# Kernel tuning notes

Measured on AMD Instinct MI355X. Metric: run time of the kernel, lower is better.

## Reference

```python
import jax, jax.numpy as jnp
import numpy as np

B, S, D, H = 2, 2048, 1024, 16
HD = D // H  # head_dim = 64


def setup_inputs() -> dict:
    key = jax.random.key(0)
    k1, k2, k3 = jax.random.split(key, 3)
    x = jax.random.normal(k1, (B, S, D), dtype=jnp.float32)
    mask = jnp.zeros((B, S, S), dtype=jnp.float32)  # additive mask
    # Dense(3*D) params (glorot-ish scale) and Dense(D) output projection
    Wqkv = jax.random.normal(k2, (D, 3 * D), dtype=jnp.float32) * (1.0 / np.sqrt(D))
    bqkv = jnp.zeros((3 * D,), dtype=jnp.float32)
    Wo = jax.random.normal(k3, (D, D), dtype=jnp.float32) * (1.0 / np.sqrt(D))
    bo = jnp.zeros((D,), dtype=jnp.float32)
    return {"x": x, "mask": mask, "Wqkv": Wqkv, "bqkv": bqkv, "Wo": Wo, "bo": bo}


def reference(x, mask, Wqkv, bqkv, Wo, bo):
    b, s, d = x.shape
    qkv = x @ Wqkv + bqkv                              # [B,S,3D]
    qkv = qkv.reshape(b, s, H, 3 * HD).transpose(0, 2, 1, 3)  # [B,H,S,3*HD]
    q, k, v = jnp.split(qkv, 3, axis=-1)               # each [B,H,S,HD]
    scale = 1.0 / jnp.sqrt(jnp.float32(HD))
    scores = jnp.einsum('bhqd,bhkd->bhqk', q, k) * scale  # [B,H,S,S]
    scores = scores + mask[:, None, :, :]
    attn = jax.nn.softmax(scores, axis=-1)
    values = jnp.einsum('bhqk,bhkd->bhqd', attn, v)    # [B,H,S,HD]
    # Faithful to original: reshape WITHOUT transposing heads back
    values = values.reshape(b, s, H * HD)              # [B,S,D]
    return values @ Wo + bo
```

## Files before the change

### kernel.cpp

```cpp
#include <hip/hip_runtime.h>
#include <hip/hip_bf16.h>

#define B_ 2
#define S_ 2048
#define D_ 1024
#define H_ 16
#define HD_ 64

typedef __attribute__((ext_vector_type(8))) short short8;
typedef __attribute__((ext_vector_type(4))) float f32x4;
typedef __attribute__((ext_vector_type(16))) float f32x16;
typedef __attribute__((ext_vector_type(4))) unsigned short us4;

static __device__ __forceinline__ ushort f2bf(float x) {
  __hip_bfloat16 h = __float2bfloat16(x);
  return *reinterpret_cast<ushort*>(&h);
}

static __device__ __forceinline__ void gld_lds16(void* lds, const void* g) {
  __builtin_amdgcn_global_load_lds(
      (__attribute__((address_space(1))) void*)(g),
      (__attribute__((address_space(3))) void*)(lds), 16, 0, 0);
}


__global__ __launch_bounds__(256) void cvt_bf16_vec(const float4* __restrict__ in,
                                                    ushort* __restrict__ out, int n4) {
  int i = blockIdx.x * blockDim.x + threadIdx.x;
  if (i < n4) {
    float4 v = in[i];
    ushort4 o;
    o.x = f2bf(v.x); o.y = f2bf(v.y); o.z = f2bf(v.z); o.w = f2bf(v.w);
    *reinterpret_cast<ushort4*>(out + (size_t)i * 4) = o;
  }
}

__global__ __launch_bounds__(256) void transpose_cvt(const float* __restrict__ in,
                                                     ushort* __restrict__ out,
                                                     int K, int N) {
  __shared__ float tile[32][33];
  const int bn = blockIdx.x * 32, bk = blockIdx.y * 32;
  const int tx = threadIdx.x, ty = threadIdx.y;
  #pragma unroll
  for (int i = ty; i < 32; i += 8)
    tile[i][tx] = in[(size_t)(bk + i) * N + bn + tx];
  __syncthreads();
  #pragma unroll
  for (int i = ty; i < 32; i += 8)
    out[(size_t)(bn + i) * K + bk + tx] = f2bf(tile[tx][i]);
}

template <bool OUT_BF16>
__global__ __launch_bounds__(256) void gemm_bt(const ushort* __restrict__ A,
                                               const ushort* __restrict__ Bt,
                                               const float* __restrict__ bias,
                                               ushort* __restrict__ Cb,
                                               float* __restrict__ Cf,
                                               int M, int N, int K) {
  __shared__ __align__(16) ushort As[128 * 32];
  __shared__ __align__(16) ushort Bs[128 * 32];
  const int tid = threadIdx.x;
  const int lane = tid & 63, wid = tid >> 6;
  const int wr = wid >> 1, wc = wid & 1;
  const int row0 = blockIdx.x * 128, col0 = blockIdx.y * 128;
  const int l15 = lane & 15, lhi = lane >> 4;

  f32x4 acc[4][4];
  #pragma unroll
  for (int i = 0; i < 4; ++i)
    #pragma unroll
    for (int j = 0; j < 4; ++j)
      acc[i][j] = f32x4{0.f, 0.f, 0.f, 0.f};

  const int sr = tid >> 2;
  const int scol = (tid & 3) * 8;

  for (int k0 = 0; k0 < K; k0 += 32) {
    gld_lds16(&As[(size_t)tid * 8],        &A[(size_t)(row0 + sr) * K + k0 + scol]);
    gld_lds16(&As[2048 + (size_t)tid * 8], &A[(size_t)(row0 + 64 + sr) * K + k0 + scol]);
    gld_lds16(&Bs[(size_t)tid * 8],        &Bt[(size_t)(col0 + sr) * K + k0 + scol]);
    gld_lds16(&Bs[2048 + (size_t)tid * 8], &Bt[(size_t)(col0 + 64 + sr) * K + k0 + scol]);
    __syncthreads();

    short8 af[4], bfr[4];
    #pragma unroll
    for (int mt = 0; mt < 4; ++mt)
      af[mt] = *(const short8*)&As[(wr * 64 + mt * 16 + l15) * 32 + lhi * 8];
    #pragma unroll
    for (int nt = 0; nt < 4; ++nt)
      bfr[nt] = *(const short8*)&Bs[(wc * 64 + nt * 16 + l15) * 32 + lhi * 8];
    #pragma unroll
    for (int mt = 0; mt < 4; ++mt)
      #pragma unroll
      for (int nt = 0; nt < 4; ++nt)
        acc[mt][nt] = __builtin_amdgcn_mfma_f32_16x16x32_bf16(af[mt], bfr[nt], acc[mt][nt], 0, 0, 0);
    __syncthreads();
  }

  const int orow = row0 + wr * 64;
  const int ocol = col0 + wc * 64 + l15;
  #pragma unroll
  for (int mt = 0; mt < 4; ++mt) {
    #pragma unroll
    for (int nt = 0; nt < 4; ++nt) {
      const int gc = ocol + nt * 16;
      const float bv = bias[gc];
      #pragma unroll
      for (int r = 0; r < 4; ++r) {
        const int gr = orow + mt * 16 + lhi * 4 + r;
        const float v = acc[mt][nt][r] + bv;
        if (OUT_BF16) Cb[(size_t)gr * N + gc] = f2bf(v);
        else          Cf[(size_t)gr * N + gc] = v;
      }
    }
  }
}

__global__ __launch_bounds__(256, 2) void flash_attn(const ushort* __restrict__ qkv,
                                                     const float* __restrict__ mask,
                                                     ushort* __restrict__ values) {
  __shared__ __align__(16) ushort Ks[2][64 * 64];
  __shared__ __align__(16) ushort Vt[2][64 * 64];

  const int tid = threadIdx.x;
  const int lane = tid & 63, wid = tid >> 6;
  const int l31 = lane & 31, lhalf = lane >> 5;
  const int qt = blockIdx.x, bh = blockIdx.y, b = bh >> 4, h = bh & 15;
  const size_t base = (size_t)b * S_ * 3072 + (size_t)h * 192;
  const int q = qt * 128 + wid * 32 + l31;
  const int NT = S_ / 64;

  short8 qf[4];
  {
    const ushort* qrow = qkv + base + (size_t)q * 3072 + lhalf * 8;
    qf[0] = *(const short8*)(qrow);
    qf[1] = *(const short8*)(qrow + 16);
    qf[2] = *(const short8*)(qrow + 32);
    qf[3] = *(const short8*)(qrow + 48);
  }

  const int srow = tid >> 3, sch = tid & 7;
  const int hsr = (srow ^ (srow >> 3)) & 7;
  const int scs = sch ^ hsr;
  const int kg = tid & 15, d0 = (tid >> 4) * 4;
  const int skg = (kg & 12) | ((kg & 1) << 1) | ((kg >> 1) & 1);

  float m_run = -3.0e38f, l_run = 0.f;
  f32x16 o[2];
  #pragma unroll
  for (int dg = 0; dg < 2; ++dg)
    #pragma unroll
    for (int i = 0; i < 16; ++i) o[dg][i] = 0.f;

  const float* mrow = mask + ((size_t)b * S_ + q) * S_;
  us4 vr[4];
  f32x16 scA[2], scB[2];

#define QKT_(SCDST, KSBUF)                                                     \
  {                                                                            \
    _Pragma("unroll")                                                          \
    for (int g = 0; g < 2; ++g) {                                              \
      const int row_ = g * 32 + l31;                                           \
      const int hk_ = (row_ ^ (row_ >> 3)) & 7;                                \
      const ushort* kp_ = &(KSBUF)[row_ * 64];                                 \
      f32x16 s_;                                                               \
      _Pragma("unroll")                                                        \
      for (int i = 0; i < 16; ++i) s_[i] = 0.f;                                \
      _Pragma("unroll")                                                        \
      for (int kd = 0; kd < 4; ++kd) {                                         \
        short8 kf_ = *(const short8*)&kp_[(((kd * 2 + lhalf) ^ hk_) & 7) * 8]; \
        s_ = __builtin_amdgcn_mfma_f32_32x32x16_bf16(kf_, qf[kd], s_, 0, 0, 0);\
      }                                                                        \
      (SCDST)[g] = s_;                                                         \
    }                                                                          \
  }

#define VSCATTER_(VTBUF)                                                       \
  {                                                                            \
    _Pragma("unroll")                                                          \
    for (int dd = 0; dd < 4; ++dd) {                                           \
      const int d_ = d0 + dd;                                                  \
      const int hd_ = (d_ ^ (d_ >> 3)) & 7;                                    \
      us4 w_;                                                                  \
      w_[0] = vr[0][dd]; w_[1] = vr[1][dd];                                    \
      w_[2] = vr[2][dd]; w_[3] = vr[3][dd];                                    \
      *(us4*)&(VTBUF)[d_ * 64 + (((skg >> 1) ^ hd_) & 7) * 8 + (skg & 1) * 4] = w_; \
    }                                                                          \
  }

#define HALF_(T, SCCUR, SCNEXT)                                                \
  {                                                                            \
    const int t_ = (T);                                                        \
    const bool pre1_ = (t_ + 1 < NT), pre2_ = (t_ + 2 < NT);                   \
    if (pre2_) {                                                               \
      const ushort* kn_ = qkv + base + (size_t)(t_ + 2) * 64 * 3072 +          \
                          (size_t)srow * 3072 + 64;                            \
      gld_lds16(&Ks[t_ & 1][tid * 8],        kn_ + scs * 8);                   \
      gld_lds16(&Ks[t_ & 1][2048 + tid * 8], kn_ + (size_t)32 * 3072 + (scs ^ 4) * 8); \
    }                                                                          \
    if (pre1_) {                                                               \
      const ushort* vn_ = qkv + base + (size_t)(t_ + 1) * 64 * 3072 + 128 + d0;\
      _Pragma("unroll")                                                        \
      for (int kk = 0; kk < 4; ++kk)                                           \
        vr[kk] = *(const us4*)(vn_ + (size_t)(kg * 4 + kk) * 3072);            \
    }                                                                          \
    f32x4 mk_[8];                                                              \
    {                                                                          \
      const float* mp_ = mrow + t_ * 64 + lhalf * 4;                           \
      _Pragma("unroll")                                                        \
      for (int i = 0; i < 8; ++i)                                              \
        mk_[i] = *(const f32x4*)(mp_ + (i >> 2) * 32 + (i & 3) * 8);           \
    }                                                                          \
    __builtin_amdgcn_s_setprio(1);                                             \
    if (pre1_) QKT_(SCNEXT, Ks[(t_ + 1) & 1]);                                 \
                     \
    _Pragma("unroll")                                                          \
    for (int g = 0; g < 2; ++g)                                                \
      _Pragma("unroll")                                                        \
      for (int r = 0; r < 16; ++r)                                             \
        (SCCUR)[g][r] = (SCCUR)[g][r] * 0.125f + mk_[g * 4 + (r >> 2)][r & 3]; \
    float mx_ = (SCCUR)[0][0];                                                 \
    _Pragma("unroll")                                                          \
    for (int g = 0; g < 2; ++g)                                                \
      _Pragma("unroll")                                                        \
      for (int r = 0; r < 16; ++r) mx_ = fmaxf(mx_, (SCCUR)[g][r]);            \
    mx_ = fmaxf(mx_, __shfl_xor(mx_, 32));                                     \
    if (__any(mx_ > m_run + 8.0f)) {                                           \
      const float mnew_ = fmaxf(m_run, mx_);                                   \
      const float alpha_ = __expf(m_run - mnew_);                              \
      m_run = mnew_;                                                           \
      l_run *= alpha_;                                                         \
      _Pragma("unroll")                                                        \
      for (int dg = 0; dg < 2; ++dg)                                           \
        _Pragma("unroll")                                                      \
        for (int i = 0; i < 16; ++i) o[dg][i] *= alpha_;                       \
    }                                                                          \
    float ps_ = 0.f;                                                           \
    _Pragma("unroll")                                                          \
    for (int g = 0; g < 2; ++g)                                                \
      _Pragma("unroll")                                                        \
      for (int r = 0; r < 16; ++r) {                                           \
        const float p_ = __expf((SCCUR)[g][r] - m_run);                        \
        (SCCUR)[g][r] = p_;                                                    \
        ps_ += p_;                                                             \
      }                                                                        \
    ps_ += __shfl_xor(ps_, 32);                                                \
    l_run += ps_;                                                              \
    short8 pf_[4];                                                             \
    _Pragma("unroll")                                                          \
    for (int ks = 0; ks < 4; ++ks)                                             \
      _Pragma("unroll")                                                        \
      for (int j = 0; j < 8; ++j)                                              \
        pf_[ks][j] = (short)f2bf((SCCUR)[ks >> 1][8 * (ks & 1) + j]);          \
    _Pragma("unroll")                                                          \
    for (int dg = 0; dg < 2; ++dg) {                                           \
      const int d_ = dg * 32 + l31;                                            \
      const int hv_ = (d_ ^ (d_ >> 3)) & 7;                                    \
      const ushort* vp_ = &Vt[t_ & 1][d_ * 64];                                \
      _Pragma("unroll")                                                        \
      for (int ks = 0; ks < 4; ++ks) {                                         \
        short8 vf_ = *(const short8*)&vp_[(((ks * 2 + lhalf) ^ hv_) & 7) * 8]; \
        o[dg] = __builtin_amdgcn_mfma_f32_32x32x16_bf16(vf_, pf_[ks], o[dg], 0, 0, 0); \
      }                                                                        \
    }                                                                          \
    __builtin_amdgcn_s_setprio(0);                                             \
    if (pre1_) VSCATTER_(Vt[(t_ + 1) & 1]);                                    \
    __syncthreads();                                                           \
  }

  {
    const ushort* k0 = qkv + base + (size_t)srow * 3072 + 64;
    gld_lds16(&Ks[0][tid * 8],        k0 + scs * 8);
    gld_lds16(&Ks[0][2048 + tid * 8], k0 + (size_t)32 * 3072 + (scs ^ 4) * 8);
    const ushort* k1 = k0 + (size_t)64 * 3072;
    gld_lds16(&Ks[1][tid * 8],        k1 + scs * 8);
    gld_lds16(&Ks[1][2048 + tid * 8], k1 + (size_t)32 * 3072 + (scs ^ 4) * 8);
    #pragma unroll
    for (int kk = 0; kk < 4; ++kk)
      vr[kk] = *(const us4*)(qkv + base + (size_t)(kg * 4 + kk) * 3072 + 128 + d0);
    VSCATTER_(Vt[0]);
    __syncthreads();
    QKT_(scA, Ks[0]);
  }

  for (int tp = 0; tp < NT; tp += 2) {
    HALF_(tp,     scA, scB);
    HALF_(tp + 1, scB, scA);
  }

  const float inv = 1.0f / l_run;
  ushort* vout = values + ((size_t)bh * S_ + q) * 64;
  #pragma unroll
  for (int dg = 0; dg < 2; ++dg)
    #pragma unroll
    for (int quad = 0; quad < 4; ++quad) {
      us4 w;
      #pragma unroll
      for (int r = 0; r < 4; ++r) w[r] = f2bf(o[dg][quad * 4 + r] * inv);
      *(us4*)(vout + dg * 32 + quad * 8 + lhalf * 4) = w;
    }
#undef HALF_
#undef VSCATTER_
#undef QKT_
}


extern "C" void kernel_launch(void* const* d_in, const int* in_sizes, int n_in,
                              void* d_out, int out_size, void* d_ws, size_t ws_size,
                              hipStream_t stream) {
  const float* x    = (const float*)d_in[0];
  const float* mask = (const float*)d_in[1];
  const float* Wqkv = (const float*)d_in[2];
  const float* bqkv = (const float*)d_in[3];
  const float* Wo   = (const float*)d_in[4];
  const float* bo   = (const float*)d_in[5];
  float* out = (float*)d_out;

  char* ws = (char*)d_ws;
  ushort* xbf    = (ushort*)(ws + 0);
  ushort* vals   = (ushort*)(ws + 0);
  ushort* wqkvT  = (ushort*)(ws + 8388608);
  ushort* woT    = (ushort*)(ws + 14680064);
  ushort* qkv    = (ushort*)(ws + 16777216);

  cvt_bf16_vec<<<4096, 256, 0, stream>>>((const float4*)x, xbf, (B_ * S_ * D_) / 4);
  transpose_cvt<<<dim3(3 * D_ / 32, D_ / 32), dim3(32, 8), 0, stream>>>(Wqkv, wqkvT, D_, 3 * D_);
  transpose_cvt<<<dim3(D_ / 32, D_ / 32), dim3(32, 8), 0, stream>>>(Wo, woT, D_, D_);
  gemm_bt<true><<<dim3((B_ * S_) / 128, (3 * D_) / 128), 256, 0, stream>>>(
      xbf, wqkvT, bqkv, qkv, nullptr, B_ * S_, 3 * D_, D_);
  flash_attn<<<dim3(S_ / 128, B_ * H_), 256, 0, stream>>>(qkv, mask, vals);
  gemm_bt<false><<<dim3((B_ * S_) / 128, D_ / 128), 256, 0, stream>>>(
      vals, woT, bo, nullptr, out, B_ * S_, D_, D_);
}
```

Measured before the change: 184.4 us.

## Fuse preprocessing kernels into one launch and swizzle GEMM workgroups across XCDs

Merges the x bf16 conversion and the two weight transpose-conversions into a single kernel that dispatches by block index, removing two kernel launches and their tail gaps. It also remaps GEMM workgroup indices so that consecutive tiles go to the same XCD, aiming for better L2 locality of the shared A/B panels. The remap assumes the workgroup count is divisible by 8.

```diff
diff --git a/kernel.cpp b/kernel.cpp
--- a/kernel.cpp
+++ b/kernel.cpp
@@ -24,23 +24,11 @@
 }
 
 
-__global__ __launch_bounds__(256) void cvt_bf16_vec(const float4* __restrict__ in,
-                                                    ushort* __restrict__ out, int n4) {
-  int i = blockIdx.x * blockDim.x + threadIdx.x;
-  if (i < n4) {
-    float4 v = in[i];
-    ushort4 o;
-    o.x = f2bf(v.x); o.y = f2bf(v.y); o.z = f2bf(v.z); o.w = f2bf(v.w);
-    *reinterpret_cast<ushort4*>(out + (size_t)i * 4) = o;
-  }
-}
-
-__global__ __launch_bounds__(256) void transpose_cvt(const float* __restrict__ in,
-                                                     ushort* __restrict__ out,
-                                                     int K, int N) {
+static __device__ __forceinline__ void transpose_tile(const float* __restrict__ in,
+                                                      ushort* __restrict__ out,
+                                                      int K, int N, int bn, int bk,
+                                                      int tx, int ty) {
   __shared__ float tile[32][33];
-  const int bn = blockIdx.x * 32, bk = blockIdx.y * 32;
-  const int tx = threadIdx.x, ty = threadIdx.y;
   #pragma unroll
   for (int i = ty; i < 32; i += 8)
     tile[i][tx] = in[(size_t)(bk + i) * N + bn + tx];
@@ -48,6 +36,30 @@
   #pragma unroll
   for (int i = ty; i < 32; i += 8)
     out[(size_t)(bn + i) * K + bk + tx] = f2bf(tile[tx][i]);
+}
+
+__global__ __launch_bounds__(256) void prep_all(const float4* __restrict__ x4,
+                                                ushort* __restrict__ xbf,
+                                                const float* __restrict__ Wqkv,
+                                                ushort* __restrict__ wqkvT,
+                                                const float* __restrict__ Wo,
+                                                ushort* __restrict__ woT) {
+  const int blk = blockIdx.x, tid = threadIdx.x;
+  if (blk < 4096) {
+    const int i = blk * 256 + tid;
+    float4 v = x4[i];
+    ushort4 o;
+    o.x = f2bf(v.x); o.y = f2bf(v.y); o.z = f2bf(v.z); o.w = f2bf(v.w);
+    *reinterpret_cast<ushort4*>(xbf + (size_t)i * 4) = o;
+  } else if (blk < 7168) {
+    const int sub = blk - 4096;
+    transpose_tile(Wqkv, wqkvT, D_, 3 * D_, (sub % 96) * 32, (sub / 96) * 32,
+                   tid & 31, tid >> 5);
+  } else {
+    const int sub = blk - 7168;
+    transpose_tile(Wo, woT, D_, D_, (sub % 32) * 32, (sub / 32) * 32,
+                   tid & 31, tid >> 5);
+  }
 }
 
 template <bool OUT_BF16>
@@ -62,7 +74,12 @@
   const int tid = threadIdx.x;
   const int lane = tid & 63, wid = tid >> 6;
   const int wr = wid >> 1, wc = wid & 1;
-  const int row0 = blockIdx.x * 128, col0 = blockIdx.y * 128;
+
+  const int nwg = gridDim.x * gridDim.y;
+  const int lin = blockIdx.x + gridDim.x * blockIdx.y;
+  const int nl = (lin & 7) * (nwg >> 3) + (lin >> 3);
+  const int row0 = (nl % gridDim.x) * 128, col0 = (nl / gridDim.x) * 128;
+
   const int l15 = lane & 15, lhi = lane >> 4;
 
   f32x4 acc[4][4];
@@ -213,7 +230,6 @@
     }                                                                          \
     __builtin_amdgcn_s_setprio(1);                                             \
     if (pre1_) QKT_(SCNEXT, Ks[(t_ + 1) & 1]);                                 \
-                     \
     _Pragma("unroll")                                                          \
     for (int g = 0; g < 2; ++g)                                                \
       _Pragma("unroll")                                                        \
@@ -323,9 +339,7 @@
   ushort* woT    = (ushort*)(ws + 14680064);
   ushort* qkv    = (ushort*)(ws + 16777216);
 
-  cvt_bf16_vec<<<4096, 256, 0, stream>>>((const float4*)x, xbf, (B_ * S_ * D_) / 4);
-  transpose_cvt<<<dim3(3 * D_ / 32, D_ / 32), dim3(32, 8), 0, stream>>>(Wqkv, wqkvT, D_, 3 * D_);
-  transpose_cvt<<<dim3(D_ / 32, D_ / 32), dim3(32, 8), 0, stream>>>(Wo, woT, D_, D_);
+  prep_all<<<8192, 256, 0, stream>>>((const float4*)x, xbf, Wqkv, wqkvT, Wo, woT);
   gemm_bt<true><<<dim3((B_ * S_) / 128, (3 * D_) / 128), 256, 0, stream>>>(
       xbf, wqkvT, bqkv, qkv, nullptr, B_ * S_, 3 * D_, D_);
   flash_attn<<<dim3(S_ / 128, B_ * H_), 256, 0, stream>>>(qkv, mask, vals);
```

Result: no change. 182.0 us (-1.3%).
